# Kernel tuning notes

Measured on AMD Instinct MI355X. Metric: run time of the kernel, lower is better.

Reference implementation:

```python
import jax, jax.numpy as jnp
import numpy as np

N_NODES = 50000
N_EDGES = 600000
IN_F, HID, OUT_F = 602, 128, 41


def _gconv(x, W, b, src, dst, n):
    # DGL GraphConv, norm='both': D_dst^{-1/2} A (D_src^{-1/2} x W) + b
    ones = jnp.ones(src.shape, dtype=x.dtype)
    deg_out = jnp.clip(jax.ops.segment_sum(ones, src, num_segments=n), 1.0)
    deg_in = jnp.clip(jax.ops.segment_sum(ones, dst, num_segments=n), 1.0)
    h = x * jax.lax.rsqrt(deg_out)[:, None]
    h = h @ W  # dense transform first (in_feats > out_feats path)
    agg = jax.ops.segment_sum(h[src], dst, num_segments=n)  # [N, out]
    return agg * jax.lax.rsqrt(deg_in)[:, None] + b


def setup_inputs() -> dict:
    key = jax.random.key(0)
    ks = jax.random.split(key, 8)
    features = jax.random.normal(ks[0], (N_NODES, IN_F), dtype=jnp.float32)
    src = jax.random.randint(ks[1], (N_EDGES,), 0, N_NODES, dtype=jnp.int32)
    dst = jax.random.randint(ks[2], (N_EDGES,), 0, N_NODES, dtype=jnp.int32)
    def glorot(k, fan_in, fan_out):
        s = jnp.sqrt(6.0 / (fan_in + fan_out)).astype(jnp.float32)
        return jax.random.uniform(k, (fan_in, fan_out), jnp.float32, -s, s)
    return {
        'features': features, 'src': src, 'dst': dst,
        'W1': glorot(ks[3], IN_F, HID), 'b1': jnp.zeros((HID,), jnp.float32),
        'W2': glorot(ks[4], HID, HID), 'b2': jnp.zeros((HID,), jnp.float32),
        'W3': glorot(ks[5], HID, HID), 'b3': jnp.zeros((HID,), jnp.float32),
        'Wfc': glorot(ks[6], HID, OUT_F), 'bfc': jnp.zeros((OUT_F,), jnp.float32),
    }


def reference(features, src, dst, W1, b1, W2, b2, W3, b3, Wfc, bfc):
    n = features.shape[0]
    relu = jax.nn.relu
    x = relu(_gconv(features, W1, b1, src, dst, n))  # x = _x
    _x = relu(_gconv(x, W2, b2, src, dst, n))        # branch (layer2)
    x = relu(_gconv(x, W2, b2, src, dst, n))         # main (same layer2)
    x = relu(_gconv(x, W3, b3, src, dst, n))         # layer3
    x = relu(x + _x)                                  # residual + relu
    return x @ Wfc + bfc
```

## Files before the change

kernel.cpp:

```cpp
#include <hip/hip_runtime.h>
#include <hip/hip_bf16.h>

#define NN   50000
#define NE   600000
#define INF  602
#define HID  128
#define OUTF 41
#define NBLK 196

typedef __attribute__((ext_vector_type(8))) short bf16x8;
typedef __attribute__((ext_vector_type(4))) float f32x4;

__device__ inline unsigned short f2bf(float x) {
    unsigned u = __float_as_uint(x);
    unsigned r = u + 0x7FFF + ((u >> 16) & 1);
    return (unsigned short)(r >> 16);
}

#define GLL16(gp, lp) \
    __builtin_amdgcn_global_load_lds((const __attribute__((address_space(1))) unsigned int*)(gp), \
                                     (__attribute__((address_space(3))) unsigned int*)(lp), 16, 0, 0)

__global__ __launch_bounds__(256) void deg_hist_k(const int* __restrict__ src,
                                                  const int* __restrict__ dst,
                                                  int* __restrict__ cnt_out,
                                                  int* __restrict__ cnt_in, int E) {
    int e = blockIdx.x * 256 + threadIdx.x;
    if (e < E) {
        atomicAdd(&cnt_out[src[e]], 1);
        atomicAdd(&cnt_in[dst[e]], 1);
    }
}

__global__ __launch_bounds__(256) void scan1_k(const int* __restrict__ cnt,
                                               int* __restrict__ rowptr,
                                               int* __restrict__ blockSum) {
    __shared__ int tmp[256];
    int tid = threadIdx.x;
    int i = blockIdx.x * 256 + tid;
    int v = (i < NN) ? cnt[i] : 0;
    tmp[tid] = v;
    __syncthreads();
#pragma unroll
    for (int off = 1; off < 256; off <<= 1) {
        int t = (tid >= off) ? tmp[tid - off] : 0;
        __syncthreads();
        tmp[tid] += t;
        __syncthreads();
    }
    if (i < NN) rowptr[i] = tmp[tid] - v;
    if (tid == 255) blockSum[blockIdx.x] = tmp[255];
}

__global__ __launch_bounds__(256) void scan2_k(const int* __restrict__ blockSum,
                                               int* __restrict__ blockOff,
                                               int* __restrict__ rowptr) {
    __shared__ int tmp[256];
    int tid = threadIdx.x;
    int v = (tid < NBLK) ? blockSum[tid] : 0;
    tmp[tid] = v;
    __syncthreads();
#pragma unroll
    for (int off = 1; off < 256; off <<= 1) {
        int t = (tid >= off) ? tmp[tid - off] : 0;
        __syncthreads();
        tmp[tid] += t;
        __syncthreads();
    }
    if (tid < NBLK) blockOff[tid] = tmp[tid] - v;
    if (tid == 255) rowptr[NN] = tmp[255];
}

__global__ __launch_bounds__(256) void scan3_k(int* __restrict__ rowptr,
                                               const int* __restrict__ blockOff,
                                               int* __restrict__ wcur,
                                               const int* __restrict__ cnt_out,
                                               const int* __restrict__ cnt_in,
                                               float* __restrict__ rs_out,
                                               float* __restrict__ rs_in) {
    int i = blockIdx.x * 256 + threadIdx.x;
    if (i < NN) {
        int r = rowptr[i] + blockOff[blockIdx.x];
        rowptr[i] = r;
        wcur[i] = r;
        int co = cnt_out[i]; if (co < 1) co = 1;
        int ci = cnt_in[i];  if (ci < 1) ci = 1;
        rs_out[i] = rsqrtf((float)co);
        rs_in[i]  = rsqrtf((float)ci);
    }
}

__global__ __launch_bounds__(256) void fill_csr_k(const int* __restrict__ src,
                                                  const int* __restrict__ dst,
                                                  int* __restrict__ wcur,
                                                  int* __restrict__ csrsrc, int E) {
    int e = blockIdx.x * 256 + threadIdx.x;
    if (e < E) {
        int p = atomicAdd(&wcur[dst[e]], 1);
        csrsrc[p] = src[e];
    }
}

__global__ __launch_bounds__(256) void prep_w_k(const float* __restrict__ W, int K,
                                                unsigned short* __restrict__ out, int total4) {
    int i = blockIdx.x * 256 + threadIdx.x;
    if (i >= total4) return;
    int col = i & 127;
    int k4 = (i >> 7) << 2;
    short4 h;
    h.x = (short)f2bf((k4 + 0 < K) ? W[(size_t)(k4 + 0) * HID + col] : 0.f);
    h.y = (short)f2bf((k4 + 1 < K) ? W[(size_t)(k4 + 1) * HID + col] : 0.f);
    h.z = (short)f2bf((k4 + 2 < K) ? W[(size_t)(k4 + 2) * HID + col] : 0.f);
    h.w = (short)f2bf((k4 + 3 < K) ? W[(size_t)(k4 + 3) * HID + col] : 0.f);
    *(short4*)&out[(size_t)(k4 >> 3) * 1024 + col * 8 + (k4 & 7)] = h;
}

__global__ __launch_bounds__(256) void gemm1_k(const float* __restrict__ A,
                                               const unsigned short* __restrict__ Wt,
                                               const float* __restrict__ rs_out,
                                               unsigned short* __restrict__ H, int n) {
    __shared__ __attribute__((aligned(16))) short As[64 * 72];
    __shared__ __attribute__((aligned(16))) short Bs[2][8192];

    const int tid = threadIdx.x;
    const int wave = tid >> 6;
    const int lane = tid & 63;
    const int quad = lane >> 4;
    const int l16 = lane & 15;
    const int wm = wave >> 1;
    const int wn = wave & 1;
    const int rowBase = blockIdx.x * 64;
    const int T = 10;

    float4 apf[4];
    auto loadA = [&](int t) {
        int kb = t << 6;
#pragma unroll
        for (int c = 0; c < 4; ++c) {
            int f = c * 256 + tid;
            int row = f >> 4;
            int col4 = (f & 15) << 2;
            int grow = rowBase + row;
            int gk = kb + col4;
            float4 v = {0.f, 0.f, 0.f, 0.f};
            if (grow < n) {
                if (gk + 3 < INF) {
                    v = *(const float4*)(A + (size_t)grow * INF + gk);
                } else {
                    if (gk + 0 < INF) v.x = A[(size_t)grow * INF + gk + 0];
                    if (gk + 1 < INF) v.y = A[(size_t)grow * INF + gk + 1];
                    if (gk + 2 < INF) v.z = A[(size_t)grow * INF + gk + 2];
                }
            }
            apf[c] = v;
        }
    };
    auto storeA = [&]() {
#pragma unroll
        for (int c = 0; c < 4; ++c) {
            int f = c * 256 + tid;
            int row = f >> 4;
            int col4 = (f & 15) << 2;
            short4 h;
            h.x = (short)f2bf(apf[c].x); h.y = (short)f2bf(apf[c].y);
            h.z = (short)f2bf(apf[c].z); h.w = (short)f2bf(apf[c].w);
            *(short4*)&As[row * 72 + col4] = h;
        }
    };
    auto issueB = [&](int t, int p) {
#pragma unroll
        for (int c = 0; c < 4; ++c)
            GLL16(Wt + (size_t)t * 8192 + c * 2048 + tid * 8, &Bs[p][c * 2048 + tid * 8]);
    };

    f32x4 acc[2][4];
#pragma unroll
    for (int i = 0; i < 2; ++i)
#pragma unroll
        for (int j = 0; j < 4; ++j) acc[i][j] = (f32x4){0.f, 0.f, 0.f, 0.f};

    loadA(0);
    issueB(0, 0);
    for (int t = 0; t < T; ++t) {
        storeA();
        __syncthreads();
        if (t + 1 < T) {
            issueB(t + 1, (t + 1) & 1);
            loadA(t + 1);
        }
        const short* B = Bs[t & 1];
#pragma unroll
        for (int kq = 0; kq < 2; ++kq) {
            bf16x8 af[2], bfr[4];
#pragma unroll
            for (int mt = 0; mt < 2; ++mt)
                af[mt] = *(const bf16x8*)&As[(wm * 32 + mt * 16 + l16) * 72 + kq * 32 + quad * 8];
#pragma unroll
            for (int nt = 0; nt < 4; ++nt)
                bfr[nt] = *(const bf16x8*)&B[(kq * 4 + quad) * 1024 + (wn * 64 + nt * 16 + l16) * 8];
#pragma unroll
            for (int mt = 0; mt < 2; ++mt)
#pragma unroll
                for (int nt = 0; nt < 4; ++nt)
                    acc[mt][nt] = __builtin_amdgcn_mfma_f32_16x16x32_bf16(af[mt], bfr[nt], acc[mt][nt], 0, 0, 0);
        }
        __syncthreads();
    }

#pragma unroll
    for (int mt = 0; mt < 2; ++mt)
#pragma unroll
        for (int r = 0; r < 4; ++r) {
            int row = rowBase + wm * 32 + mt * 16 + quad * 4 + r;
            if (row < n) {
                float ro = rs_out[row];
#pragma unroll
                for (int nt = 0; nt < 4; ++nt) {
                    int col = wn * 64 + nt * 16 + l16;
                    H[(size_t)row * HID + col] = f2bf(acc[mt][nt][r] * ro);
                }
            }
        }
}

__global__ __launch_bounds__(256) void gemm_hid_k(const unsigned short* __restrict__ A,
                                                  const unsigned short* __restrict__ Wt,
                                                  unsigned short* __restrict__ H, int n) {
    __shared__ __attribute__((aligned(16))) short As[64 * 136];
    __shared__ __attribute__((aligned(16))) short Bs[16384];

    const int tid = threadIdx.x;
    const int wave = tid >> 6;
    const int lane = tid & 63;
    const int quad = lane >> 4;
    const int l16 = lane & 15;
    const int wm = wave >> 1;
    const int wn = wave & 1;
    const int rowBase = blockIdx.x * 64;

#pragma unroll
    for (int c = 0; c < 8; ++c)
        GLL16(Wt + c * 2048 + tid * 8, &Bs[c * 2048 + tid * 8]);

#pragma unroll
    for (int c = 0; c < 4; ++c) {
        int f = c * 256 + tid;
        int row = f >> 4;
        int k16 = (f & 15) << 3;
        int grow = rowBase + row;
        int4 v = {0, 0, 0, 0};
        if (grow < n) v = *(const int4*)(A + (size_t)grow * HID + k16);
        *(int4*)&As[row * 136 + k16] = v;
    }
    __syncthreads();

    f32x4 acc[2][4];
#pragma unroll
    for (int i = 0; i < 2; ++i)
#pragma unroll
        for (int j = 0; j < 4; ++j) acc[i][j] = (f32x4){0.f, 0.f, 0.f, 0.f};

#pragma unroll
    for (int kq = 0; kq < 4; ++kq) {
        bf16x8 af[2], bfr[4];
#pragma unroll
        for (int mt = 0; mt < 2; ++mt)
            af[mt] = *(const bf16x8*)&As[(wm * 32 + mt * 16 + l16) * 136 + kq * 32 + quad * 8];
#pragma unroll
        for (int nt = 0; nt < 4; ++nt)
            bfr[nt] = *(const bf16x8*)&Bs[(kq * 4 + quad) * 1024 + (wn * 64 + nt * 16 + l16) * 8];
#pragma unroll
        for (int mt = 0; mt < 2; ++mt)
#pragma unroll
            for (int nt = 0; nt < 4; ++nt)
                acc[mt][nt] = __builtin_amdgcn_mfma_f32_16x16x32_bf16(af[mt], bfr[nt], acc[mt][nt], 0, 0, 0);
    }

#pragma unroll
    for (int mt = 0; mt < 2; ++mt)
#pragma unroll
        for (int r = 0; r < 4; ++r) {
            int row = rowBase + wm * 32 + mt * 16 + quad * 4 + r;
            if (row < n) {
#pragma unroll
                for (int nt = 0; nt < 4; ++nt) {
                    int col = wn * 64 + nt * 16 + l16;
                    H[(size_t)row * HID + col] = f2bf(acc[mt][nt][r]);
                }
            }
        }
}

__global__ __launch_bounds__(256) void gather_k(const unsigned short* __restrict__ H,
                                                const int* __restrict__ rowptr,
                                                const int* __restrict__ csrsrc,
                                                const float* __restrict__ rs_in,
                                                const float* __restrict__ rs_out,
                                                const float* __restrict__ bias,
                                                const float* __restrict__ resid,
                                                float* __restrict__ outX,
                                                unsigned short* __restrict__ outXs,
                                                int n) {
    int node = blockIdx.x * 4 + (threadIdx.x >> 6);
    if (node >= n) return;
    int lane = threadIdx.x & 63;
    const unsigned int* Hu = (const unsigned int*)H;
    int beg = rowptr[node], end = rowptr[node + 1];
    float ax = 0.f, ay = 0.f, bx2 = 0.f, by2 = 0.f;
    int p = beg;
    for (; p + 1 < end; p += 2) {
        unsigned u0 = Hu[(size_t)csrsrc[p] * 64 + lane];
        unsigned u1 = Hu[(size_t)csrsrc[p + 1] * 64 + lane];
        ax += __uint_as_float(u0 << 16);
        ay += __uint_as_float(u0 & 0xFFFF0000u);
        bx2 += __uint_as_float(u1 << 16);
        by2 += __uint_as_float(u1 & 0xFFFF0000u);
    }
    if (p < end) {
        unsigned u = Hu[(size_t)csrsrc[p] * 64 + lane];
        ax += __uint_as_float(u << 16);
        ay += __uint_as_float(u & 0xFFFF0000u);
    }
    ax += bx2; ay += by2;
    float ri = rs_in[node];
    float vx = fmaxf(ax * ri + bias[lane * 2], 0.f);
    float vy = fmaxf(ay * ri + bias[lane * 2 + 1], 0.f);
    if (resid) {
        float2 r = *(const float2*)(resid + (size_t)node * HID + lane * 2);
        vx = fmaxf(vx + r.x, 0.f);
        vy = fmaxf(vy + r.y, 0.f);
    }
    size_t o = (size_t)node * HID + lane * 2;
    if (outX) { *(float2*)(outX + o) = make_float2(vx, vy); }
    if (outXs) {
        float ro = rs_out[node];
        ushort2 h;
        h.x = f2bf(vx * ro);
        h.y = f2bf(vy * ro);
        *(ushort2*)(outXs + o) = h;
    }
}

__global__ __launch_bounds__(256) void fc_k(const float* __restrict__ X,
                                            const float* __restrict__ Wfc,
                                            const float* __restrict__ bfc,
                                            float* __restrict__ out, int n) {
    __shared__ float Ws[HID * OUTF];
    __shared__ float Xs[4][HID];
    int tid = threadIdx.x;
    for (int i = tid; i < HID * OUTF; i += 256) Ws[i] = Wfc[i];
    int rowBase = blockIdx.x * 4;
    for (int i = tid; i < 4 * HID; i += 256) {
        int r = i >> 7, c = i & 127;
        int gr = rowBase + r;
        Xs[r][c] = (gr < n) ? X[(size_t)gr * HID + c] : 0.f;
    }
    __syncthreads();
    int wv = tid >> 6, lane = tid & 63;
    int row = rowBase + wv;
    if (row < n && lane < OUTF) {
        float acc = bfc[lane];
#pragma unroll 8
        for (int k = 0; k < HID; ++k) acc += Xs[wv][k] * Ws[k * OUTF + lane];
        out[(size_t)row * OUTF + lane] = acc;
    }
}

extern "C" void kernel_launch(void* const* d_in, const int* in_sizes, int n_in,
                              void* d_out, int out_size, void* d_ws, size_t ws_size,
                              hipStream_t stream) {
    const float* feat = (const float*)d_in[0];
    const int* src = (const int*)d_in[1];
    const int* dst = (const int*)d_in[2];
    const float* W1 = (const float*)d_in[3];
    const float* b1 = (const float*)d_in[4];
    const float* W2 = (const float*)d_in[5];
    const float* b2 = (const float*)d_in[6];
    const float* W3 = (const float*)d_in[7];
    const float* b3 = (const float*)d_in[8];
    const float* Wfc = (const float*)d_in[9];
    const float* bfc = (const float*)d_in[10];
    float* out = (float*)d_out;

    char* w = (char*)d_ws;
    auto alloc = [&](size_t b) -> void* {
        void* p = (void*)w;
        w += (b + 255) & ~(size_t)255;
        return p;
    };
    int* cnt_out = (int*)alloc(NN * sizeof(int));
    int* cnt_in  = (int*)alloc(NN * sizeof(int));
    int* rowptr  = (int*)alloc((NN + 1) * sizeof(int));
    int* wcur    = (int*)alloc(NN * sizeof(int));
    int* csrsrc  = (int*)alloc(NE * sizeof(int));
    int* blockSum = (int*)alloc(NBLK * sizeof(int));
    int* blockOff = (int*)alloc(NBLK * sizeof(int));
    float* rs_out = (float*)alloc(NN * sizeof(float));
    float* rs_in  = (float*)alloc(NN * sizeof(float));
    unsigned short* W1t = (unsigned short*)alloc(10 * 8192 * sizeof(unsigned short));
    unsigned short* W2t = (unsigned short*)alloc(16384 * sizeof(unsigned short));
    unsigned short* W3t = (unsigned short*)alloc(16384 * sizeof(unsigned short));
    unsigned short* Hb = (unsigned short*)alloc((size_t)NN * HID * sizeof(unsigned short));
    unsigned short* Xb = (unsigned short*)alloc((size_t)NN * HID * sizeof(unsigned short));
    float* resid = (float*)alloc((size_t)NN * HID * sizeof(float));
    float* Xfc   = (float*)alloc((size_t)NN * HID * sizeof(float));

    hipMemsetAsync(cnt_out, 0, NN * sizeof(int), stream);
    hipMemsetAsync(cnt_in, 0, NN * sizeof(int), stream);

    prep_w_k<<<80, 256, 0, stream>>>(W1, INF, W1t, 20480);
    prep_w_k<<<16, 256, 0, stream>>>(W2, HID, W2t, 4096);
    prep_w_k<<<16, 256, 0, stream>>>(W3, HID, W3t, 4096);

    deg_hist_k<<<(NE + 255) / 256, 256, 0, stream>>>(src, dst, cnt_out, cnt_in, NE);
    scan1_k<<<NBLK, 256, 0, stream>>>(cnt_in, rowptr, blockSum);
    scan2_k<<<1, 256, 0, stream>>>(blockSum, blockOff, rowptr);
    scan3_k<<<NBLK, 256, 0, stream>>>(rowptr, blockOff, wcur, cnt_out, cnt_in, rs_out, rs_in);
    fill_csr_k<<<(NE + 255) / 256, 256, 0, stream>>>(src, dst, wcur, csrsrc, NE);

    const int gblk = (NN + 63) / 64;
    gemm1_k<<<gblk, 256, 0, stream>>>(feat, W1t, rs_out, Hb, NN);
    gather_k<<<(NN + 3) / 4, 256, 0, stream>>>(Hb, rowptr, csrsrc, rs_in, rs_out, b1,
                                               nullptr, nullptr, Xb, NN);
    gemm_hid_k<<<gblk, 256, 0, stream>>>(Xb, W2t, Hb, NN);
    gather_k<<<(NN + 3) / 4, 256, 0, stream>>>(Hb, rowptr, csrsrc, rs_in, rs_out, b2,
                                               nullptr, resid, Xb, NN);
    gemm_hid_k<<<gblk, 256, 0, stream>>>(Xb, W3t, Hb, NN);
    gather_k<<<(NN + 3) / 4, 256, 0, stream>>>(Hb, rowptr, csrsrc, rs_in, rs_out, b3,
                                               resid, Xfc, nullptr, NN);
    fc_k<<<(NN + 3) / 4, 256, 0, stream>>>(Xfc, Wfc, bfc, out, NN);
}
```

Baseline: 517.0 us.

## Drop LDS staging in GEMM kernels; load MFMA operands directly from global

Both dense GEMM kernels stop staging A and the weight tile through shared memory with barriers. Each wave now owns 16 rows and all 128 output columns. It loads its A fragment straight from global, converting fp32 to bf16 in registers for the first layer, and reads B fragments directly from the pre-swizzled weight buffer, which should mostly hit in cache. This removes LDS traffic, __syncthreads and the double-buffer bookkeeping. The cost is losing A reuse across waves in a block, B fragments re-read per wave from L1/L2, and a handwritten tail path for K=602.

```diff
diff --git a/kernel.cpp b/kernel.cpp
--- a/kernel.cpp
+++ b/kernel.cpp
@@ -17,9 +17,14 @@
     return (unsigned short)(r >> 16);
 }
 
-#define GLL16(gp, lp) \
-    __builtin_amdgcn_global_load_lds((const __attribute__((address_space(1))) unsigned int*)(gp), \
-                                     (__attribute__((address_space(3))) unsigned int*)(lp), 16, 0, 0)
+__device__ inline bf16x8 cvt8(float4 a0, float4 a1) {
+    bf16x8 h;
+    h[0] = (short)f2bf(a0.x); h[1] = (short)f2bf(a0.y);
+    h[2] = (short)f2bf(a0.z); h[3] = (short)f2bf(a0.w);
+    h[4] = (short)f2bf(a1.x); h[5] = (short)f2bf(a1.y);
+    h[6] = (short)f2bf(a1.z); h[7] = (short)f2bf(a1.w);
+    return h;
+}
 
 __global__ __launch_bounds__(256) void deg_hist_k(const int* __restrict__ src,
                                                   const int* __restrict__ dst,
@@ -119,176 +124,105 @@
                                                const unsigned short* __restrict__ Wt,
                                                const float* __restrict__ rs_out,
                                                unsigned short* __restrict__ H, int n) {
-    __shared__ __attribute__((aligned(16))) short As[64 * 72];
-    __shared__ __attribute__((aligned(16))) short Bs[2][8192];
-
     const int tid = threadIdx.x;
     const int wave = tid >> 6;
     const int lane = tid & 63;
     const int quad = lane >> 4;
     const int l16 = lane & 15;
-    const int wm = wave >> 1;
-    const int wn = wave & 1;
-    const int rowBase = blockIdx.x * 64;
-    const int T = 10;
-
-    float4 apf[4];
-    auto loadA = [&](int t) {
-        int kb = t << 6;
-#pragma unroll
-        for (int c = 0; c < 4; ++c) {
-            int f = c * 256 + tid;
-            int row = f >> 4;
-            int col4 = (f & 15) << 2;
-            int grow = rowBase + row;
-            int gk = kb + col4;
-            float4 v = {0.f, 0.f, 0.f, 0.f};
-            if (grow < n) {
-                if (gk + 3 < INF) {
-                    v = *(const float4*)(A + (size_t)grow * INF + gk);
-                } else {
-                    if (gk + 0 < INF) v.x = A[(size_t)grow * INF + gk + 0];
-                    if (gk + 1 < INF) v.y = A[(size_t)grow * INF + gk + 1];
-                    if (gk + 2 < INF) v.z = A[(size_t)grow * INF + gk + 2];
-                }
+    const int tileBase = blockIdx.x * 64 + wave * 16;
+    const int arow_i = tileBase + l16;
+    const bool rv = arow_i < n;
+    const float* arow = A + (size_t)arow_i * INF;
+
+    f32x4 acc[8];
+#pragma unroll
+    for (int j = 0; j < 8; ++j) acc[j] = (f32x4){0.f, 0.f, 0.f, 0.f};
+
+    for (int t = 0; t < 18; ++t) {
+        int k0 = t * 32 + quad * 8;
+        float4 a0 = {0.f, 0.f, 0.f, 0.f}, a1 = {0.f, 0.f, 0.f, 0.f};
+        if (rv) {
+            a0 = *(const float4*)(arow + k0);
+            a1 = *(const float4*)(arow + k0 + 4);
+        }
+        bf16x8 af = cvt8(a0, a1);
+        const unsigned short* bg = Wt + (size_t)(t * 4 + quad) * 1024 + l16 * 8;
+#pragma unroll
+        for (int nt = 0; nt < 8; ++nt) {
+            bf16x8 bf = *(const bf16x8*)(bg + nt * 128);
+            acc[nt] = __builtin_amdgcn_mfma_f32_16x16x32_bf16(af, bf, acc[nt], 0, 0, 0);
+        }
+    }
+    {
+        float4 a0 = {0.f, 0.f, 0.f, 0.f}, a1 = {0.f, 0.f, 0.f, 0.f};
+        if (rv) {
+            int k0 = 576 + quad * 8;
+            if (quad < 3) {
+                a0 = *(const float4*)(arow + k0);
+                a1 = *(const float4*)(arow + k0 + 4);
+            } else {
+                a0.x = arow[600];
+                a0.y = arow[601];
             }
-            apf[c] = v;
-        }
-    };
-    auto storeA = [&]() {
-#pragma unroll
-        for (int c = 0; c < 4; ++c) {
-            int f = c * 256 + tid;
-            int row = f >> 4;
-            int col4 = (f & 15) << 2;
-            short4 h;
-            h.x = (short)f2bf(apf[c].x); h.y = (short)f2bf(apf[c].y);
-            h.z = (short)f2bf(apf[c].z); h.w = (short)f2bf(apf[c].w);
-            *(short4*)&As[row * 72 + col4] = h;
-        }
-    };
-    auto issueB = [&](int t, int p) {
-#pragma unroll
-        for (int c = 0; c < 4; ++c)
-            GLL16(Wt + (size_t)t * 8192 + c * 2048 + tid * 8, &Bs[p][c * 2048 + tid * 8]);
-    };
-
-    f32x4 acc[2][4];
-#pragma unroll
-    for (int i = 0; i < 2; ++i)
-#pragma unroll
-        for (int j = 0; j < 4; ++j) acc[i][j] = (f32x4){0.f, 0.f, 0.f, 0.f};
-
-    loadA(0);
-    issueB(0, 0);
-    for (int t = 0; t < T; ++t) {
-        storeA();
-        __syncthreads();
-        if (t + 1 < T) {
-            issueB(t + 1, (t + 1) & 1);
-            loadA(t + 1);
-        }
-        const short* B = Bs[t & 1];
-#pragma unroll
-        for (int kq = 0; kq < 2; ++kq) {
-            bf16x8 af[2], bfr[4];
-#pragma unroll
-            for (int mt = 0; mt < 2; ++mt)
-                af[mt] = *(const bf16x8*)&As[(wm * 32 + mt * 16 + l16) * 72 + kq * 32 + quad * 8];
-#pragma unroll
-            for (int nt = 0; nt < 4; ++nt)
-                bfr[nt] = *(const bf16x8*)&B[(kq * 4 + quad) * 1024 + (wn * 64 + nt * 16 + l16) * 8];
-#pragma unroll
-            for (int mt = 0; mt < 2; ++mt)
-#pragma unroll
-                for (int nt = 0; nt < 4; ++nt)
-                    acc[mt][nt] = __builtin_amdgcn_mfma_f32_16x16x32_bf16(af[mt], bfr[nt], acc[mt][nt], 0, 0, 0);
-        }
-        __syncthreads();
-    }
-
-#pragma unroll
-    for (int mt = 0; mt < 2; ++mt)
-#pragma unroll
-        for (int r = 0; r < 4; ++r) {
-            int row = rowBase + wm * 32 + mt * 16 + quad * 4 + r;
-            if (row < n) {
-                float ro = rs_out[row];
-#pragma unroll
-                for (int nt = 0; nt < 4; ++nt) {
-                    int col = wn * 64 + nt * 16 + l16;
-                    H[(size_t)row * HID + col] = f2bf(acc[mt][nt][r] * ro);
-                }
-            }
-        }
+        }
+        bf16x8 af = cvt8(a0, a1);
+        const unsigned short* bg = Wt + (size_t)(18 * 4 + quad) * 1024 + l16 * 8;
+#pragma unroll
+        for (int nt = 0; nt < 8; ++nt) {
+            bf16x8 bf = *(const bf16x8*)(bg + nt * 128);
+            acc[nt] = __builtin_amdgcn_mfma_f32_16x16x32_bf16(af, bf, acc[nt], 0, 0, 0);
+        }
+    }
+
+#pragma unroll
+    for (int r = 0; r < 4; ++r) {
+        int row = tileBase + quad * 4 + r;
+        if (row < n) {
+            float ro = rs_out[row];
+#pragma unroll
+            for (int nt = 0; nt < 8; ++nt)
+                H[(size_t)row * HID + nt * 16 + l16] = f2bf(acc[nt][r] * ro);
+        }
+    }
 }
 
 __global__ __launch_bounds__(256) void gemm_hid_k(const unsigned short* __restrict__ A,
                                                   const unsigned short* __restrict__ Wt,
                                                   unsigned short* __restrict__ H, int n) {
-    __shared__ __attribute__((aligned(16))) short As[64 * 136];
-    __shared__ __attribute__((aligned(16))) short Bs[16384];
-
     const int tid = threadIdx.x;
     const int wave = tid >> 6;
     const int lane = tid & 63;
     const int quad = lane >> 4;
     const int l16 = lane & 15;
-    const int wm = wave >> 1;
-    const int wn = wave & 1;
-    const int rowBase = blockIdx.x * 64;
-
-#pragma unroll
-    for (int c = 0; c < 8; ++c)
-        GLL16(Wt + c * 2048 + tid * 8, &Bs[c * 2048 + tid * 8]);
-
-#pragma unroll
-    for (int c = 0; c < 4; ++c) {
-        int f = c * 256 + tid;
-        int row = f >> 4;
-        int k16 = (f & 15) << 3;
-        int grow = rowBase + row;
-        int4 v = {0, 0, 0, 0};
-        if (grow < n) v = *(const int4*)(A + (size_t)grow * HID + k16);
-        *(int4*)&As[row * 136 + k16] = v;
-    }
-    __syncthreads();
-
-    f32x4 acc[2][4];
-#pragma unroll
-    for (int i = 0; i < 2; ++i)
-#pragma unroll
-        for (int j = 0; j < 4; ++j) acc[i][j] = (f32x4){0.f, 0.f, 0.f, 0.f};
-
-#pragma unroll
-    for (int kq = 0; kq < 4; ++kq) {
-        bf16x8 af[2], bfr[4];
-#pragma unroll
-        for (int mt = 0; mt < 2; ++mt)
-            af[mt] = *(const bf16x8*)&As[(wm * 32 + mt * 16 + l16) * 136 + kq * 32 + quad * 8];
-#pragma unroll
-        for (int nt = 0; nt < 4; ++nt)
-            bfr[nt] = *(const bf16x8*)&Bs[(kq * 4 + quad) * 1024 + (wn * 64 + nt * 16 + l16) * 8];
-#pragma unroll
-        for (int mt = 0; mt < 2; ++mt)
-#pragma unroll
-            for (int nt = 0; nt < 4; ++nt)
-                acc[mt][nt] = __builtin_amdgcn_mfma_f32_16x16x32_bf16(af[mt], bfr[nt], acc[mt][nt], 0, 0, 0);
-    }
-
-#pragma unroll
-    for (int mt = 0; mt < 2; ++mt)
-#pragma unroll
-        for (int r = 0; r < 4; ++r) {
-            int row = rowBase + wm * 32 + mt * 16 + quad * 4 + r;
-            if (row < n) {
-#pragma unroll
-                for (int nt = 0; nt < 4; ++nt) {
-                    int col = wn * 64 + nt * 16 + l16;
-                    H[(size_t)row * HID + col] = f2bf(acc[mt][nt][r]);
-                }
-            }
-        }
+    const int tileBase = blockIdx.x * 64 + wave * 16;
+    const int arow_i = tileBase + l16;
+    const bool rv = arow_i < n;
+
+    f32x4 acc[8];
+#pragma unroll
+    for (int j = 0; j < 8; ++j) acc[j] = (f32x4){0.f, 0.f, 0.f, 0.f};
+
+#pragma unroll 2
+    for (int t = 0; t < 4; ++t) {
+        bf16x8 af = (bf16x8){0, 0, 0, 0, 0, 0, 0, 0};
+        if (rv) af = *(const bf16x8*)(A + (size_t)arow_i * HID + t * 32 + quad * 8);
+        const unsigned short* bg = Wt + (size_t)(t * 4 + quad) * 1024 + l16 * 8;
+#pragma unroll
+        for (int nt = 0; nt < 8; ++nt) {
+            bf16x8 bf = *(const bf16x8*)(bg + nt * 128);
+            acc[nt] = __builtin_amdgcn_mfma_f32_16x16x32_bf16(af, bf, acc[nt], 0, 0, 0);
+        }
+    }
+
+#pragma unroll
+    for (int r = 0; r < 4; ++r) {
+        int row = tileBase + quad * 4 + r;
+        if (row < n) {
+#pragma unroll
+            for (int nt = 0; nt < 8; ++nt)
+                H[(size_t)row * HID + nt * 16 + l16] = f2bf(acc[nt][r]);
+        }
+    }
 }
 
 __global__ __launch_bounds__(256) void gather_k(const unsigned short* __restrict__ H,
```

After: 525.9 us. About the same (+1.7%).

## Restructure layer-1 GEMM into 128-wide K chunks with per-wave 16-row tiles

Applied to the files above, without the earlier changes.

The first-layer GEMM now walks K in five 128-wide chunks instead of ten 64-wide steps, and B is loaded into a single 16K-element LDS buffer instead of being double-buffered. Each wave owns a 16-row strip and covers all 128 output columns, so one A fragment is reused across eight MFMAs. This halves the number of barrier rounds per tile but drops the overlap between the next B load and the current compute, since B is issued right before a sync. The weight matrix must still be padded to a multiple of 128 in K (5×128=640 ≥ 602).

```diff
diff --git a/kernel.cpp b/kernel.cpp
--- a/kernel.cpp
+++ b/kernel.cpp
@@ -119,29 +119,27 @@
                                                const unsigned short* __restrict__ Wt,
                                                const float* __restrict__ rs_out,
                                                unsigned short* __restrict__ H, int n) {
-    __shared__ __attribute__((aligned(16))) short As[64 * 72];
-    __shared__ __attribute__((aligned(16))) short Bs[2][8192];
+    __shared__ __attribute__((aligned(16))) short As[64 * 136];
+    __shared__ __attribute__((aligned(16))) short Bs[16 * 1024];
 
     const int tid = threadIdx.x;
     const int wave = tid >> 6;
     const int lane = tid & 63;
     const int quad = lane >> 4;
     const int l16 = lane & 15;
-    const int wm = wave >> 1;
-    const int wn = wave & 1;
     const int rowBase = blockIdx.x * 64;
-    const int T = 10;
-
-    float4 apf[4];
-    auto loadA = [&](int t) {
-        int kb = t << 6;
-#pragma unroll
-        for (int c = 0; c < 4; ++c) {
+    const int tileBase = rowBase + wave * 16;
+
+    float4 apf[8];
+    auto loadA = [&](int ch) {
+        int kb = ch * 128;
+#pragma unroll
+        for (int c = 0; c < 8; ++c) {
             int f = c * 256 + tid;
-            int row = f >> 4;
-            int col4 = (f & 15) << 2;
+            int row = f >> 5;
+            int kc = (f & 31) << 2;
             int grow = rowBase + row;
-            int gk = kb + col4;
+            int gk = kb + kc;
             float4 v = {0.f, 0.f, 0.f, 0.f};
             if (grow < n) {
                 if (gk + 3 < INF) {
@@ -157,70 +155,55 @@
     };
     auto storeA = [&]() {
 #pragma unroll
-        for (int c = 0; c < 4; ++c) {
+        for (int c = 0; c < 8; ++c) {
             int f = c * 256 + tid;
-            int row = f >> 4;
-            int col4 = (f & 15) << 2;
+            int row = f >> 5;
+            int kc = (f & 31) << 2;
             short4 h;
             h.x = (short)f2bf(apf[c].x); h.y = (short)f2bf(apf[c].y);
             h.z = (short)f2bf(apf[c].z); h.w = (short)f2bf(apf[c].w);
-            *(short4*)&As[row * 72 + col4] = h;
+            *(short4*)&As[row * 136 + kc] = h;
         }
     };
-    auto issueB = [&](int t, int p) {
-#pragma unroll
-        for (int c = 0; c < 4; ++c)
-            GLL16(Wt + (size_t)t * 8192 + c * 2048 + tid * 8, &Bs[p][c * 2048 + tid * 8]);
+    auto issueB = [&](int ch) {
+#pragma unroll
+        for (int c = 0; c < 8; ++c)
+            GLL16(Wt + (size_t)ch * 16384 + c * 2048 + tid * 8, &Bs[c * 2048 + tid * 8]);
     };
 
-    f32x4 acc[2][4];
-#pragma unroll
-    for (int i = 0; i < 2; ++i)
-#pragma unroll
-        for (int j = 0; j < 4; ++j) acc[i][j] = (f32x4){0.f, 0.f, 0.f, 0.f};
+    f32x4 acc[8];
+#pragma unroll
+    for (int j = 0; j < 8; ++j) acc[j] = (f32x4){0.f, 0.f, 0.f, 0.f};
 
     loadA(0);
-    issueB(0, 0);
-    for (int t = 0; t < T; ++t) {
+    for (int ch = 0; ch < 5; ++ch) {
+        __syncthreads();
+        issueB(ch);
         storeA();
         __syncthreads();
-        if (t + 1 < T) {
-            issueB(t + 1, (t + 1) & 1);
-            loadA(t + 1);
-        }
-        const short* B = Bs[t & 1];
-#pragma unroll
-        for (int kq = 0; kq < 2; ++kq) {
-            bf16x8 af[2], bfr[4];
-#pragma unroll
-            for (int mt = 0; mt < 2; ++mt)
-                af[mt] = *(const bf16x8*)&As[(wm * 32 + mt * 16 + l16) * 72 + kq * 32 + quad * 8];
-#pragma unroll
-            for (int nt = 0; nt < 4; ++nt)
-                bfr[nt] = *(const bf16x8*)&B[(kq * 4 + quad) * 1024 + (wn * 64 + nt * 16 + l16) * 8];
-#pragma unroll
-            for (int mt = 0; mt < 2; ++mt)
-#pragma unroll
-                for (int nt = 0; nt < 4; ++nt)
-                    acc[mt][nt] = __builtin_amdgcn_mfma_f32_16x16x32_bf16(af[mt], bfr[nt], acc[mt][nt], 0, 0, 0);
-        }
-        __syncthreads();
-    }
-
-#pragma unroll
-    for (int mt = 0; mt < 2; ++mt)
-#pragma unroll
-        for (int r = 0; r < 4; ++r) {
-            int row = rowBase + wm * 32 + mt * 16 + quad * 4 + r;
-            if (row < n) {
-                float ro = rs_out[row];
-#pragma unroll
-                for (int nt = 0; nt < 4; ++nt) {
-                    int col = wn * 64 + nt * 16 + l16;
-                    H[(size_t)row * HID + col] = f2bf(acc[mt][nt][r] * ro);
-                }
+        if (ch + 1 < 5) loadA(ch + 1);
+#pragma unroll
+        for (int s = 0; s < 4; ++s) {
+            bf16x8 af = *(const bf16x8*)&As[(wave * 16 + l16) * 136 + s * 32 + quad * 8];
+            const short* bg = &Bs[(s * 4 + quad) * 1024 + l16 * 8];
+#pragma unroll
+            for (int nt = 0; nt < 8; ++nt) {
+                bf16x8 bf = *(const bf16x8*)(bg + nt * 128);
+                acc[nt] = __builtin_amdgcn_mfma_f32_16x16x32_bf16(af, bf, acc[nt], 0, 0, 0);
             }
         }
+    }
+
+#pragma unroll
+    for (int r = 0; r < 4; ++r) {
+        int row = tileBase + quad * 4 + r;
+        if (row < n) {
+            float ro = rs_out[row];
+#pragma unroll
+            for (int nt = 0; nt < 8; ++nt)
+                H[(size_t)row * HID + nt * 16 + l16] = f2bf(acc[nt][r] * ro);
+        }
+    }
 }
 
 __global__ __launch_bounds__(256) void gemm_hid_k(const unsigned short* __restrict__ A,
```

Result: no change. 514.3 us (-0.5%).
